# Performance work log

Measured on AMD Instinct MI355X. Metric: run time of the kernel, lower is better.

## Reference

```python
import jax, jax.numpy as jnp
import numpy as np

B, K, D = 8, 4000, 256
H, DQ, DV = 8, 32, 32
WIN, PAD = 200, 50
STEP = WIN - 2 * PAD  # 100
BETA = 0.25


def setup_inputs() -> dict:
    key = jax.random.key(0)
    ks = jax.random.split(key, 14)
    s = 0.02
    return {
        "query": jax.random.normal(ks[0], (B, K, D), jnp.float32),
        "key": jax.random.normal(ks[1], (B, K, D), jnp.float32),
        "value": jax.random.normal(ks[2], (B, K, D), jnp.float32),
        "Wq": jax.random.normal(ks[3], (D, H * DQ), jnp.float32) * s,
        "bq": jax.random.normal(ks[4], (H * DQ,), jnp.float32) * s,
        "Wk": jax.random.normal(ks[5], (D, H * DQ), jnp.float32) * s,
        "bk": jax.random.normal(ks[6], (H * DQ,), jnp.float32) * s,
        "Wv": jax.random.normal(ks[7], (D, H * DV), jnp.float32) * s,
        "bv": jax.random.normal(ks[8], (H * DV,), jnp.float32) * s,
        "Wo": jax.random.normal(ks[9], (H * DV, D), jnp.float32) * s,
        "bo": jax.random.normal(ks[10], (D,), jnp.float32) * s,
    }


def _windows(x, n_win):
    starts = jnp.arange(n_win) * STEP
    idx = starts[:, None] + jnp.arange(WIN)[None, :]
    return x[:, :, idx, :]


def reference(query, key, value, Wq, bq, Wk, bk, Wv, bv, Wo, bo):
    b, k_len, d = query.shape
    pad = lambda t: jnp.pad(t, ((0, 0), (PAD, PAD), (0, 0)), mode='edge')  # replicate pad
    qp, kp, vp = pad(query), pad(key), pad(value)
    kpad = k_len + 2 * PAD
    n_win = (kpad - WIN) // STEP + 1

    def proj(x, Wm, bias, dh):
        y = x @ Wm + bias                       # [B, Kp, H*dh]
        return y.reshape(b, kpad, H, dh).transpose(0, 2, 1, 3)  # [B, H, Kp, dh]

    q = _windows(proj(qp, Wq, bq, DQ), n_win)
    kk = _windows(proj(kp, Wk, bk, DQ), n_win)
    v = _windows(proj(vp, Wv, bv, DV), n_win)

    scores = jnp.einsum('bhnid,bhnjd->bhnij', q, kk) / jnp.sqrt(jnp.float32(WIN))
    dist = jnp.abs(jnp.arange(WIN)[:, None] - jnp.arange(WIN)[None, :]).astype(scores.dtype)
    cauchy = (1.0 / (1.0 + BETA * dist * dist)) * (1.0 - jnp.eye(WIN, dtype=scores.dtype))
    scores = scores * cauchy
    causal = jnp.triu(jnp.ones((WIN, WIN), dtype=bool), k=1)  # attention_size is not None -> causal masking
    scores = jnp.where(causal, -jnp.inf, scores)
    attn = jax.nn.softmax(scores, axis=-1)
    out = jnp.einsum('bhnij,bhnjd->bhnid', attn, v)
    out = out[:, :, :, PAD:WIN - PAD, :].reshape(b, H, k_len, DV)
    out = out.transpose(0, 2, 1, 3).reshape(b, k_len, H * DV)  # heads concatenated, head-major slices
    return out @ Wo + bo
```

## Files before the change

kernel.cpp:

```cpp
#include <hip/hip_runtime.h>


typedef __bf16 bf16_t;
typedef __bf16 bf16x8 __attribute__((ext_vector_type(8)));
typedef float  f32x4  __attribute__((ext_vector_type(4)));

#define MFMA16(a, b, c) __builtin_amdgcn_mfma_f32_16x16x32_bf16((a), (b), (c), 0, 0, 0)

typedef __attribute__((address_space(1))) const unsigned char gas_u8;
typedef __attribute__((address_space(3))) unsigned char las_u8;

static __device__ __forceinline__ void gload16(const void* g, void* l) {
  __builtin_amdgcn_global_load_lds((gas_u8*)g, (las_u8*)l, 16, 0, 0);
}

static __device__ __forceinline__ bf16x8 cvt8(float4 a, float4 b) {
  bf16x8 r;
  r[0] = (bf16_t)a.x; r[1] = (bf16_t)a.y; r[2] = (bf16_t)a.z; r[3] = (bf16_t)a.w;
  r[4] = (bf16_t)b.x; r[5] = (bf16_t)b.y; r[6] = (bf16_t)b.z; r[7] = (bf16_t)b.w;
  return r;
}

static __device__ __forceinline__ unsigned short bbits(bf16_t v) {
  union { bf16_t b; unsigned short u; } c; c.b = v; return c.u;
}

__global__ __launch_bounds__(256)
void prep_weights(const float* __restrict__ Wq, const float* __restrict__ Wk,
                  const float* __restrict__ Wv, const float* __restrict__ Wo,
                  bf16_t* __restrict__ wt) {
  const int mat  = blockIdx.x >> 6;
  const int tile = blockIdx.x & 63;
  const int kt = (tile >> 3) * 32, nt = (tile & 7) * 32;
  const float* W = (mat == 0) ? Wq : (mat == 1) ? Wk : (mat == 2) ? Wv : Wo;
  __shared__ float t[32][33];
  const int tx = threadIdx.x & 31, ty = threadIdx.x >> 5;
#pragma unroll
  for (int i = 0; i < 32; i += 8)
    t[ty + i][tx] = W[(size_t)(kt + ty + i) * 256 + nt + tx];
  __syncthreads();
  bf16_t* dst = wt + (size_t)mat * 65536;
#pragma unroll
  for (int i = 0; i < 32; i += 8)
    dst[(size_t)(nt + ty + i) * 256 + kt + tx] = (bf16_t)t[tx][ty + i];
}

template <int MODE>
__global__ __launch_bounds__(512)
void gemm5(const void* __restrict__ Xv, const bf16_t* __restrict__ W,
           const float* __restrict__ bias, void* __restrict__ Out, int M,
           float oscale) {
  constexpr bool INB = (MODE == 3);
  __shared__ __align__(16) char ldsB[2 * 16384];

  const int tid  = threadIdx.x;
  const int lane = tid & 63;
  const int w    = tid >> 6;
  const int wm   = (w & 3) * 16;
  const int wn   = (w >> 2) * 128;
  const int lo   = lane & 15, hi = lane >> 4;
  const int m0   = blockIdx.x * 64;

  int ar = m0 + wm + lo; if (ar >= M) ar = M - 1;
  bf16x8 areg[8];
  if constexpr (!INB) {
    const float4* ap = (const float4*)((const float*)Xv + (size_t)ar * 256);
#pragma unroll
    for (int t = 0; t < 8; ++t)
      areg[t] = cvt8(ap[t * 8 + hi * 2], ap[t * 8 + hi * 2 + 1]);
  } else {
    const bf16_t* ap = (const bf16_t*)Xv + (size_t)ar * 256;
#pragma unroll
    for (int t = 0; t < 8; ++t)
      areg[t] = *(const bf16x8*)(ap + t * 32 + hi * 8);
  }

  const bf16_t* bsrc[2];
  int boff[2];
#pragma unroll
  for (int j = 0; j < 2; ++j) {
    const int s = j * 512 + tid;
    bsrc[j] = W + (size_t)(s >> 2) * 256 + ((s & 3) << 3);
    boff[j] = s * 16;
  }
  int bbase[8];
#pragma unroll
  for (int ni = 0; ni < 8; ++ni)
    bbase[ni] = (wn + ni * 16 + lo) * 64 + hi * 16;

#pragma unroll
  for (int j = 0; j < 2; ++j) gload16(bsrc[j], ldsB + boff[j]);

  f32x4 acc[8] = {};

  for (int t = 0; t < 8; ++t) {
    const int cur = (t & 1) * 16384;
    if (t < 7) {
      const int nxt = ((t + 1) & 1) * 16384;
#pragma unroll
      for (int j = 0; j < 2; ++j) gload16(bsrc[j] + (t + 1) * 32, ldsB + nxt + boff[j]);
      asm volatile("s_waitcnt vmcnt(2)" ::: "memory");
    } else {
      asm volatile("s_waitcnt vmcnt(0)" ::: "memory");
    }
    __builtin_amdgcn_sched_barrier(0);
    __builtin_amdgcn_s_barrier();

#pragma unroll
    for (int ni = 0; ni < 8; ++ni) {
      const bf16x8 bfv = *(const bf16x8*)(ldsB + cur + bbase[ni]);
      acc[ni] = MFMA16(areg[t], bfv, acc[ni]);
    }
    __builtin_amdgcn_sched_barrier(0);
    __builtin_amdgcn_s_barrier();
  }

  const int mb = m0 + wm + hi * 4;
  if (mb >= M) return;
#pragma unroll
  for (int ni = 0; ni < 8; ++ni) {
    const int n = wn + ni * 16 + lo;
    const float bia = bias[n];
    if constexpr (MODE == 0) {
      bf16_t* O = (bf16_t*)Out;
#pragma unroll
      for (int rr = 0; rr < 4; ++rr)
        O[(size_t)(mb + rr) * 256 + n] = (bf16_t)((acc[ni][rr] + bia) * oscale);
    } else if constexpr (MODE == 1) {
      const int b = mb / 4000, t = mb - b * 4000;
      bf16_t* O = (bf16_t*)Out;
#pragma unroll
      for (int rr = 0; rr < 4; ++rr) {
        const bf16_t v = (bf16_t)(acc[ni][rr] + bia);
        O[((size_t)b * 4064 + t + 50 + rr) * 256 + n] = v;
        if (t == 0 && rr == 0)
          for (int p = 0; p < 50; ++p)
            O[((size_t)b * 4064 + p) * 256 + n] = v;
      }
    } else if constexpr (MODE == 2) {
      const int b = mb / 4000, t = mb - b * 4000;
      const size_t vrow = ((size_t)(b * 256 + n)) * 4064;
      bf16_t* O = (bf16_t*)Out;
      unsigned short e0 = bbits((bf16_t)(acc[ni][0] + bia));
      unsigned short e1 = bbits((bf16_t)(acc[ni][1] + bia));
      unsigned short e2 = bbits((bf16_t)(acc[ni][2] + bia));
      unsigned short e3 = bbits((bf16_t)(acc[ni][3] + bia));
      unsigned* O32 = (unsigned*)(O + vrow + t + 50);
      O32[0] = (unsigned)e0 | ((unsigned)e1 << 16);
      O32[1] = (unsigned)e2 | ((unsigned)e3 << 16);
      if (t == 0) {
        const unsigned vv = (unsigned)e0 | ((unsigned)e0 << 16);
        unsigned* P = (unsigned*)(O + vrow);
#pragma unroll
        for (int p = 0; p < 25; ++p) P[p] = vv;
      }
    } else {
      float* O = (float*)Out;
#pragma unroll
      for (int rr = 0; rr < 4; ++rr)
        O[(size_t)(mb + rr) * 256 + n] = acc[ni][rr] + bia;
    }
  }
}

__global__ __launch_bounds__(448)
void attn_win(const bf16_t* __restrict__ qb, const bf16_t* __restrict__ kb,
              const bf16_t* __restrict__ vt, bf16_t* __restrict__ ao) {
  const int blk = blockIdx.x;
  const int n = blk % 40;
  const int h = (blk / 40) & 7;
  const int b = blk / 320;
  const int wv = threadIdx.x >> 6;
  const int lane = threadIdx.x & 63;
  const int lo = lane & 15, hi = lane >> 4;

  __shared__ __align__(16) bf16_t E[7][16][40];

  const int i0 = 50 + 16 * wv;
  int jtmax = (65 + 16 * wv) >> 4;
  if (jtmax > 9) jtmax = 9;
  const int reach = jtmax * 16 + 16;

  int tq = n * 100 + 16 * wv + lo;
  if (tq > 3999) tq = 3999;
  const bf16x8 qf = *(const bf16x8*)&qb[((size_t)b * 4000 + tq) * 256 + h * 32 + hi * 8];

  const f32x4 zero = {0.f, 0.f, 0.f, 0.f};
  bf16x8 onesf;
#pragma unroll
  for (int u = 0; u < 8; ++u) onesf[u] = (bf16_t)1.0f;

  f32x4 o0 = zero, o1 = zero, sm = zero;
  const size_t vbase = ((size_t)(b * 256 + h * 32)) * 4064 + n * 100;
  const size_t kbase = ((size_t)(b * 4064 + n * 100)) * 256 + h * 32 + hi * 8;
  const int dbase = i0 + hi * 4 - lo;

#pragma unroll
  for (int kt = 0; kt < 5; ++kt) if (kt * 32 < reach) {
#pragma unroll
    for (int half = 0; half < 2; ++half) {
      const int jt = kt * 2 + half;
      if (jt <= jtmax) {
        const bf16x8 kf = *(const bf16x8*)&kb[kbase + (size_t)(jt * 16 + lo) * 256];
        const f32x4 s = MFMA16(qf, kf, zero);
#pragma unroll
        for (int r = 0; r < 4; ++r) {
          const int d = dbase + r - jt * 16;
          const float df = (float)d;
          float c = __builtin_amdgcn_rcpf(__builtin_fmaf(0.25f * df, df, 1.f));
          c = (d == 0) ? 0.f : c;
          float e = __expf(s[r] * c);
          e = (d < 0) ? 0.f : e;
          E[wv][hi * 4 + r][half * 16 + lo] = (bf16_t)e;
        }
      } else {
#pragma unroll
        for (int r = 0; r < 4; ++r)
          E[wv][hi * 4 + r][half * 16 + lo] = (bf16_t)0.f;
      }
    }
    const bf16x8 pf = *(const bf16x8*)&E[wv][lo][hi * 8];
    const bf16x8 v0 = *(const bf16x8*)&vt[vbase + (size_t)lo * 4064 + kt * 32 + hi * 8];
    const bf16x8 v1 = *(const bf16x8*)&vt[vbase + (size_t)(16 + lo) * 4064 + kt * 32 + hi * 8];
    o0 = MFMA16(pf, v0, o0);
    o1 = MFMA16(pf, v1, o1);
    sm = MFMA16(pf, onesf, sm);
  }

#pragma unroll
  for (int r = 0; r < 4; ++r) {
    const int i = i0 + hi * 4 + r;
    if (i < 150) {
      const float ri = __builtin_amdgcn_rcpf(sm[r]);
      const int t = n * 100 + i - 50;
      bf16_t* op = &ao[((size_t)b * 4000 + t) * 256 + h * 32];
      op[lo]      = (bf16_t)(o0[r] * ri);
      op[16 + lo] = (bf16_t)(o1[r] * ri);
    }
  }
}

extern "C" void kernel_launch(void* const* d_in, const int* in_sizes, int n_in,
                              void* d_out, int out_size, void* d_ws, size_t ws_size,
                              hipStream_t stream) {
  (void)in_sizes; (void)n_in; (void)out_size;
  const float* query = (const float*)d_in[0];
  const float* key   = (const float*)d_in[1];
  const float* value = (const float*)d_in[2];
  const float* Wq = (const float*)d_in[3];
  const float* bq = (const float*)d_in[4];
  const float* Wk = (const float*)d_in[5];
  const float* bk = (const float*)d_in[6];
  const float* Wv = (const float*)d_in[7];
  const float* bv = (const float*)d_in[8];
  const float* Wo = (const float*)d_in[9];
  const float* bo = (const float*)d_in[10];

  int bc = 8;
  while (bc > 1 && 524288ull + (unsigned long long)bc * 8257536ull > (unsigned long long)ws_size)
    bc >>= 1;

  bf16_t* wt = (bf16_t*)d_ws;
  bf16_t* qb = wt + 4 * 65536;
  bf16_t* kb = qb + (size_t)bc * 4000 * 256;
  bf16_t* vt = kb + (size_t)bc * 4064 * 256;
  bf16_t* ao = vt + (size_t)bc * 256 * 4064;

  prep_weights<<<256, 256, 0, stream>>>(Wq, Wk, Wv, Wo, wt);

  const float qscale = 0.07071067811865475f;

  for (int b0 = 0; b0 < 8; b0 += bc) {
    const int M = bc * 4000;
    const int mblk = (M + 63) / 64;
    const float* qx = query + (size_t)b0 * 4000 * 256;
    const float* kx = key   + (size_t)b0 * 4000 * 256;
    const float* vx = value + (size_t)b0 * 4000 * 256;
    float* ox = (float*)d_out + (size_t)b0 * 4000 * 256;

    gemm5<0><<<mblk, 512, 0, stream>>>(qx, wt + 0 * 65536, bq, qb, M, qscale);
    gemm5<1><<<mblk, 512, 0, stream>>>(kx, wt + 1 * 65536, bk, kb, M, 1.f);
    gemm5<2><<<mblk, 512, 0, stream>>>(vx, wt + 2 * 65536, bv, vt, M, 1.f);
    attn_win<<<bc * 320, 448, 0, stream>>>(qb, kb, vt, ao);
    gemm5<3><<<mblk, 512, 0, stream>>>(ao, wt + 3 * 65536, bo, ox, M, 1.f);
  }
}
```

Before: 114.7 us.

## Stage A tiles via LDS with register-blocked 4x4 MFMA GEMM and separate V transpose

The projection GEMM is rebuilt to use 256 threads, with 4x4 MFMA register blocking per wave. A tiles now stream through double-buffered, XOR-swizzled LDS using global_load_lds instead of being preloaded into registers. The K projection is written unpadded, and attention clamps key indices itself. The V projection now writes row-major output, and a new vtrans kernel produces the padded transposed layout, trading the scattered transposed stores for an extra pass and a larger workspace.

```diff
diff --git a/kernel.cpp b/kernel.cpp
--- a/kernel.cpp
+++ b/kernel.cpp
@@ -45,126 +45,175 @@
     dst[(size_t)(nt + ty + i) * 256 + kt + tx] = (bf16_t)t[tx][ty + i];
 }
 
-template <int MODE>
-__global__ __launch_bounds__(512)
-void gemm5(const void* __restrict__ Xv, const bf16_t* __restrict__ W,
+template <int INF32, int OUTF32>
+__global__ __launch_bounds__(256)
+void gemmR(const void* __restrict__ Xv, const bf16_t* __restrict__ W,
            const float* __restrict__ bias, void* __restrict__ Out, int M,
            float oscale) {
-  constexpr bool INB = (MODE == 3);
-  __shared__ __align__(16) char ldsB[2 * 16384];
+  constexpr int ASZ = INF32 ? 8192 : 4096;
+  constexpr int STRIDE = ASZ + 16384;
+  __shared__ __align__(16) char lds[2 * STRIDE];
 
   const int tid  = threadIdx.x;
   const int lane = tid & 63;
   const int w    = tid >> 6;
-  const int wm   = (w & 3) * 16;
-  const int wn   = (w >> 2) * 128;
   const int lo   = lane & 15, hi = lane >> 4;
   const int m0   = blockIdx.x * 64;
 
-  int ar = m0 + wm + lo; if (ar >= M) ar = M - 1;
-  bf16x8 areg[8];
-  if constexpr (!INB) {
-    const float4* ap = (const float4*)((const float*)Xv + (size_t)ar * 256);
-#pragma unroll
-    for (int t = 0; t < 8; ++t)
-      areg[t] = cvt8(ap[t * 8 + hi * 2], ap[t * 8 + hi * 2 + 1]);
+  const void* asrc[2];
+  int aoff[2];
+  if constexpr (INF32) {
+#pragma unroll
+    for (int j = 0; j < 2; ++j) {
+      const int s = j * 256 + tid;
+      const int row = s >> 3, cs = s & 7;
+      int ar = m0 + row; if (ar >= M) ar = M - 1;
+      asrc[j] = (const float*)Xv + (size_t)ar * 256 + ((cs ^ (row & 7)) << 2);
+      aoff[j] = s * 16;
+    }
   } else {
-    const bf16_t* ap = (const bf16_t*)Xv + (size_t)ar * 256;
-#pragma unroll
-    for (int t = 0; t < 8; ++t)
-      areg[t] = *(const bf16x8*)(ap + t * 32 + hi * 8);
-  }
-
-  const bf16_t* bsrc[2];
-  int boff[2];
-#pragma unroll
-  for (int j = 0; j < 2; ++j) {
-    const int s = j * 512 + tid;
+    const int s = tid;
+    const int row = s >> 2, cs = s & 3;
+    int ar = m0 + row; if (ar >= M) ar = M - 1;
+    asrc[0] = (const bf16_t*)Xv + (size_t)ar * 256 + ((cs ^ (row & 3)) << 3);
+    aoff[0] = s * 16;
+    asrc[1] = asrc[0]; aoff[1] = aoff[0];
+  }
+  const bf16_t* bsrc[4];
+  int boff[4];
+#pragma unroll
+  for (int j = 0; j < 4; ++j) {
+    const int s = j * 256 + tid;
     bsrc[j] = W + (size_t)(s >> 2) * 256 + ((s & 3) << 3);
-    boff[j] = s * 16;
-  }
-  int bbase[8];
-#pragma unroll
-  for (int ni = 0; ni < 8; ++ni)
-    bbase[ni] = (wn + ni * 16 + lo) * 64 + hi * 16;
-
-#pragma unroll
-  for (int j = 0; j < 2; ++j) gload16(bsrc[j], ldsB + boff[j]);
-
-  f32x4 acc[8] = {};
+    boff[j] = ASZ + s * 16;
+  }
+  int bbase[4];
+#pragma unroll
+  for (int ni = 0; ni < 4; ++ni)
+    bbase[ni] = ASZ + (w * 64 + ni * 16 + lo) * 64 + hi * 16;
+
+  if constexpr (INF32) {
+    gload16(asrc[0], lds + aoff[0]);
+    gload16((const float*)asrc[1], lds + aoff[1]);
+  } else {
+    gload16(asrc[0], lds + aoff[0]);
+  }
+#pragma unroll
+  for (int j = 0; j < 4; ++j) gload16(bsrc[j], lds + boff[j]);
+
+  f32x4 acc[4][4] = {};
 
   for (int t = 0; t < 8; ++t) {
-    const int cur = (t & 1) * 16384;
+    const int cur = (t & 1) * STRIDE;
     if (t < 7) {
-      const int nxt = ((t + 1) & 1) * 16384;
-#pragma unroll
-      for (int j = 0; j < 2; ++j) gload16(bsrc[j] + (t + 1) * 32, ldsB + nxt + boff[j]);
-      asm volatile("s_waitcnt vmcnt(2)" ::: "memory");
+      const int nxt = ((t + 1) & 1) * STRIDE;
+      if constexpr (INF32) {
+        gload16((const float*)asrc[0] + (t + 1) * 32, lds + nxt + aoff[0]);
+        gload16((const float*)asrc[1] + (t + 1) * 32, lds + nxt + aoff[1]);
+      } else {
+        gload16((const bf16_t*)asrc[0] + (t + 1) * 32, lds + nxt + aoff[0]);
+      }
+#pragma unroll
+      for (int j = 0; j < 4; ++j)
+        gload16(bsrc[j] + (t + 1) * 32, lds + nxt + boff[j]);
+      if constexpr (INF32) {
+        asm volatile("s_waitcnt vmcnt(6)" ::: "memory");
+      } else {
+        asm volatile("s_waitcnt vmcnt(5)" ::: "memory");
+      }
     } else {
       asm volatile("s_waitcnt vmcnt(0)" ::: "memory");
     }
     __builtin_amdgcn_sched_barrier(0);
     __builtin_amdgcn_s_barrier();
 
-#pragma unroll
-    for (int ni = 0; ni < 8; ++ni) {
-      const bf16x8 bfv = *(const bf16x8*)(ldsB + cur + bbase[ni]);
-      acc[ni] = MFMA16(areg[t], bfv, acc[ni]);
-    }
+    bf16x8 af[4], bfv[4];
+#pragma unroll
+    for (int mi = 0; mi < 4; ++mi) {
+      const int r = mi * 16 + lo;
+      if constexpr (INF32) {
+        const int ab = cur + r * 128 + (((2 * hi) ^ (r & 7)) << 4);
+        const float4 v0 = *(const float4*)(lds + ab);
+        const float4 v1 = *(const float4*)(lds + (ab ^ 16));
+        af[mi] = cvt8(v0, v1);
+      } else {
+        const int ab = cur + r * 64 + ((hi ^ (r & 3)) << 4);
+        af[mi] = *(const bf16x8*)(lds + ab);
+      }
+    }
+#pragma unroll
+    for (int ni = 0; ni < 4; ++ni)
+      bfv[ni] = *(const bf16x8*)(lds + cur + bbase[ni]);
+#pragma unroll
+    for (int mi = 0; mi < 4; ++mi)
+#pragma unroll
+      for (int ni = 0; ni < 4; ++ni)
+        acc[mi][ni] = MFMA16(af[mi], bfv[ni], acc[mi][ni]);
     __builtin_amdgcn_sched_barrier(0);
     __builtin_amdgcn_s_barrier();
   }
 
-  const int mb = m0 + wm + hi * 4;
-  if (mb >= M) return;
-#pragma unroll
-  for (int ni = 0; ni < 8; ++ni) {
-    const int n = wn + ni * 16 + lo;
-    const float bia = bias[n];
-    if constexpr (MODE == 0) {
-      bf16_t* O = (bf16_t*)Out;
-#pragma unroll
-      for (int rr = 0; rr < 4; ++rr)
-        O[(size_t)(mb + rr) * 256 + n] = (bf16_t)((acc[ni][rr] + bia) * oscale);
-    } else if constexpr (MODE == 1) {
-      const int b = mb / 4000, t = mb - b * 4000;
-      bf16_t* O = (bf16_t*)Out;
-#pragma unroll
-      for (int rr = 0; rr < 4; ++rr) {
-        const bf16_t v = (bf16_t)(acc[ni][rr] + bia);
-        O[((size_t)b * 4064 + t + 50 + rr) * 256 + n] = v;
-        if (t == 0 && rr == 0)
-          for (int p = 0; p < 50; ++p)
-            O[((size_t)b * 4064 + p) * 256 + n] = v;
-      }
-    } else if constexpr (MODE == 2) {
-      const int b = mb / 4000, t = mb - b * 4000;
-      const size_t vrow = ((size_t)(b * 256 + n)) * 4064;
-      bf16_t* O = (bf16_t*)Out;
-      unsigned short e0 = bbits((bf16_t)(acc[ni][0] + bia));
-      unsigned short e1 = bbits((bf16_t)(acc[ni][1] + bia));
-      unsigned short e2 = bbits((bf16_t)(acc[ni][2] + bia));
-      unsigned short e3 = bbits((bf16_t)(acc[ni][3] + bia));
-      unsigned* O32 = (unsigned*)(O + vrow + t + 50);
-      O32[0] = (unsigned)e0 | ((unsigned)e1 << 16);
-      O32[1] = (unsigned)e2 | ((unsigned)e3 << 16);
-      if (t == 0) {
-        const unsigned vv = (unsigned)e0 | ((unsigned)e0 << 16);
-        unsigned* P = (unsigned*)(O + vrow);
-#pragma unroll
-        for (int p = 0; p < 25; ++p) P[p] = vv;
-      }
-    } else {
-      float* O = (float*)Out;
-#pragma unroll
-      for (int rr = 0; rr < 4; ++rr)
-        O[(size_t)(mb + rr) * 256 + n] = acc[ni][rr] + bia;
-    }
+#pragma unroll
+  for (int mi = 0; mi < 4; ++mi) {
+    const int mb = m0 + mi * 16 + hi * 4;
+    if (mb >= M) continue;
+#pragma unroll
+    for (int ni = 0; ni < 4; ++ni) {
+      const int n = w * 64 + ni * 16 + lo;
+      const float bia = bias[n];
+      if constexpr (OUTF32) {
+        float* O = (float*)Out;
+#pragma unroll
+        for (int rr = 0; rr < 4; ++rr)
+          O[(size_t)(mb + rr) * 256 + n] = acc[mi][ni][rr] + bia;
+      } else {
+        bf16_t* O = (bf16_t*)Out;
+#pragma unroll
+        for (int rr = 0; rr < 4; ++rr)
+          O[(size_t)(mb + rr) * 256 + n] = (bf16_t)((acc[mi][ni][rr] + bia) * oscale);
+      }
+    }
+  }
+}
+
+__global__ __launch_bounds__(256)
+void vtrans(const bf16_t* __restrict__ vb, bf16_t* __restrict__ vt) {
+  const int t0 = blockIdx.x * 64, n0 = blockIdx.y * 64, b = blockIdx.z;
+  __shared__ bf16_t T[64][72];
+  const int tid = threadIdx.x;
+#pragma unroll
+  for (int u = 0; u < 2; ++u) {
+    const int s = u * 256 + tid;
+    const int row = s >> 3, cc = s & 7;
+    int t = t0 + row; if (t > 3999) t = 3999;
+    const bf16x8 v = *(const bf16x8*)&vb[((size_t)b * 4000 + t) * 256 + n0 + cc * 8];
+#pragma unroll
+    for (int e = 0; e < 8; ++e) T[cc * 8 + e][row] = v[e];
+  }
+  __syncthreads();
+#pragma unroll
+  for (int u = 0; u < 2; ++u) {
+    const int s = u * 256 + tid;
+    const int nr = s >> 3, cc = s & 7;
+    const int tb = t0 + cc * 8;
+    bf16_t* dst = vt + ((size_t)b * 256 + n0 + nr) * 4064 + 50 + tb;
+    const bf16_t* src = &T[nr][cc * 8];
+#pragma unroll
+    for (int e = 0; e < 4; ++e)
+      if (tb + 2 * e < 4000)
+        ((unsigned*)dst)[e] = ((const unsigned*)src)[e];
+  }
+  if (blockIdx.x == 0 && tid < 64) {
+    const unsigned short e = bbits(T[tid][0]);
+    const unsigned vv = (unsigned)e | ((unsigned)e << 16);
+    unsigned* P = (unsigned*)(vt + ((size_t)b * 256 + n0 + tid) * 4064);
+#pragma unroll
+    for (int p = 0; p < 25; ++p) P[p] = vv;
   }
 }
 
 __global__ __launch_bounds__(448)
-void attn_win(const bf16_t* __restrict__ qb, const bf16_t* __restrict__ kb,
+void attn_win(const bf16_t* __restrict__ qb, const bf16_t* __restrict__ kr,
               const bf16_t* __restrict__ vt, bf16_t* __restrict__ ao) {
   const int blk = blockIdx.x;
   const int n = blk % 40;
@@ -192,7 +241,6 @@
 
   f32x4 o0 = zero, o1 = zero, sm = zero;
   const size_t vbase = ((size_t)(b * 256 + h * 32)) * 4064 + n * 100;
-  const size_t kbase = ((size_t)(b * 4064 + n * 100)) * 256 + h * 32 + hi * 8;
   const int dbase = i0 + hi * 4 - lo;
 
 #pragma unroll
@@ -201,7 +249,9 @@
     for (int half = 0; half < 2; ++half) {
       const int jt = kt * 2 + half;
       if (jt <= jtmax) {
-        const bf16x8 kf = *(const bf16x8*)&kb[kbase + (size_t)(jt * 16 + lo) * 256];
+        int tk = n * 100 + jt * 16 + lo - 50;
+        tk = (tk < 0) ? 0 : (tk > 3999 ? 3999 : tk);
+        const bf16x8 kf = *(const bf16x8*)&kr[((size_t)b * 4000 + tk) * 256 + h * 32 + hi * 8];
         const f32x4 s = MFMA16(qf, kf, zero);
 #pragma unroll
         for (int r = 0; r < 4; ++r) {
@@ -257,13 +307,14 @@
   const float* bo = (const float*)d_in[10];
 
   int bc = 8;
-  while (bc > 1 && 524288ull + (unsigned long long)bc * 8257536ull > (unsigned long long)ws_size)
+  while (bc > 1 && 524288ull + (unsigned long long)bc * 10272768ull > (unsigned long long)ws_size)
     bc >>= 1;
 
   bf16_t* wt = (bf16_t*)d_ws;
   bf16_t* qb = wt + 4 * 65536;
-  bf16_t* kb = qb + (size_t)bc * 4000 * 256;
-  bf16_t* vt = kb + (size_t)bc * 4064 * 256;
+  bf16_t* kr = qb + (size_t)bc * 4000 * 256;
+  bf16_t* vb = kr + (size_t)bc * 4000 * 256;
+  bf16_t* vt = vb + (size_t)bc * 4000 * 256;
   bf16_t* ao = vt + (size_t)bc * 256 * 4064;
 
   prep_weights<<<256, 256, 0, stream>>>(Wq, Wk, Wv, Wo, wt);
@@ -278,10 +329,11 @@
     const float* vx = value + (size_t)b0 * 4000 * 256;
     float* ox = (float*)d_out + (size_t)b0 * 4000 * 256;
 
-    gemm5<0><<<mblk, 512, 0, stream>>>(qx, wt + 0 * 65536, bq, qb, M, qscale);
-    gemm5<1><<<mblk, 512, 0, stream>>>(kx, wt + 1 * 65536, bk, kb, M, 1.f);
-    gemm5<2><<<mblk, 512, 0, stream>>>(vx, wt + 2 * 65536, bv, vt, M, 1.f);
-    attn_win<<<bc * 320, 448, 0, stream>>>(qb, kb, vt, ao);
-    gemm5<3><<<mblk, 512, 0, stream>>>(ao, wt + 3 * 65536, bo, ox, M, 1.f);
-  }
-}
+    gemmR<1, 0><<<mblk, 256, 0, stream>>>(qx, wt + 0 * 65536, bq, qb, M, qscale);
+    gemmR<1, 0><<<mblk, 256, 0, stream>>>(kx, wt + 1 * 65536, bk, kr, M, 1.f);
+    gemmR<1, 0><<<mblk, 256, 0, stream>>>(vx, wt + 2 * 65536, bv, vb, M, 1.f);
+    vtrans<<<dim3(63, 4, bc), 256, 0, stream>>>(vb, vt);
+    attn_win<<<bc * 320, 448, 0, stream>>>(qb, kr, vt, ao);
+    gemmR<0, 1><<<mblk, 256, 0, stream>>>(ao, wt + 3 * 65536, bo, ox, M, 1.f);
+  }
+}
```

After: 110.3 us. 3.8% less time.
